# Kernel tuning notes

Hardware: AMD Instinct MI355X
Metric: run time of the kernel (lower is better)

Reference implementation:

```python
import jax, jax.numpy as jnp
import numpy as np

B, N, T, S, H = 8, 10000, 2000, 12, 128
BIN_SIGMA = 0.1
GAUSS_NORM = 0.3989422804  # 1/sqrt(2*pi), as hard-coded in the source


def setup_inputs() -> dict:
    key = jax.random.key(0)
    ks = jax.random.split(key, 8)
    # (x, y, z): x,y in detector mm, z already expressed in waveform-tick units
    scale = jnp.array([400.0, 400.0, float(T - 1)], dtype=jnp.float32)
    diffused_electrons = jax.random.uniform(ks[0], (B, N, 3), dtype=jnp.float32) * scale
    mask = jax.random.uniform(ks[1], (B, N), dtype=jnp.float32)  # per-electron weights
    W1 = jax.random.normal(ks[2], (3, H), dtype=jnp.float32) * (1.0 / np.sqrt(3.0))
    b1 = jnp.zeros((H,), dtype=jnp.float32)
    W2 = jax.random.normal(ks[3], (H, H), dtype=jnp.float32) * (1.0 / np.sqrt(H))
    b2 = jnp.zeros((H,), dtype=jnp.float32)
    W3 = jax.random.normal(ks[4], (H, S), dtype=jnp.float32) * (1.0 / np.sqrt(H))
    b3 = jnp.zeros((S,), dtype=jnp.float32)
    return {"diffused_electrons": diffused_electrons, "mask": mask,
            "W1": W1, "b1": b1, "W2": W2, "b2": b2, "W3": W3, "b3": b3}


def _mlp(x, W1, b1, W2, b2, W3, b3):
    h = jax.nn.relu(x @ W1 + b1)
    h = jaxax = jax.nn.relu(h @ W2 + b2)
    return h @ W3 + b3


def reference(diffused_electrons, mask, W1, b1, W2, b2, W3, b3):
    # sensor_simulator: per-electron sensor response [B, N, S]
    h = jax.nn.relu(diffused_electrons @ W1 + b1)
    h = jax.nn.relu(h @ W2 + b2)
    response = h @ W3 + b3  # [B, N, S]

    z = diffused_electrons[:, :, 2]  # [B, N]
    ticks = jnp.arange(T, dtype=diffused_electrons.dtype)  # linspace(0, T-1, T)
    # Gaussian soft-binning kernel, [B, N, T] (the large HBM intermediate)
    d = ticks[None, None, :] - z[:, :, None]
    exp_values = jnp.exp(-(d * d) / (2.0 * BIN_SIGMA))
    exp_values = exp_values * (mask * (GAUSS_NORM / np.sqrt(BIN_SIGMA)))[:, :, None]
    # transpose().matmul(sensor_response) then transpose -> [B, S, T]
    waveforms = jnp.einsum('bnt,bns->bst', exp_values, response)
    return waveforms
```

## Files before the change

### kernel.cpp

```cpp
#include <hip/hip_runtime.h>
#include <hip/hip_fp16.h>

#define BB 8
#define NN 10000
#define TT 2000
#define SS 12
#define HH 128
#define TOTAL_E (BB * NN)
#define COEF 1.2615662610100802f

#define CAP 32
#define REC_F 16

#define WS_CURSOR 0
#define WS_REC    65536

typedef _Float16 half8 __attribute__((ext_vector_type(8)));
typedef float f32x4 __attribute__((ext_vector_type(4)));

__device__ __forceinline__ int swz(int row, int chunk) {
    return row * 128 + ((chunk ^ (row & 7)) * 8);
}

__global__ __launch_bounds__(256) void mlp_kernel(
    const float* __restrict__ de,
    const float* __restrict__ mask,
    const float* __restrict__ W1, const float* __restrict__ b1,
    const float* __restrict__ W2, const float* __restrict__ b2,
    const float* __restrict__ W3, const float* __restrict__ b3,
    unsigned int* __restrict__ cursor,
    float* __restrict__ rec)
{
    __shared__ _Float16 sW2T[HH * 128];
    __shared__ _Float16 sh[64 * 128];

    const int tid = threadIdx.x;
    const int wave = tid >> 6;
    const int lane = tid & 63;
    const int q = lane >> 4;
    const int i = lane & 15;

    {
        const int n = tid >> 1;
        const int kh = (tid & 1) * 8;
        #pragma unroll
        for (int c8 = 0; c8 < 8; ++c8) {
            const int c = kh + c8;
            half8 v;
            #pragma unroll
            for (int j = 0; j < 8; ++j)
                v[j] = (_Float16)W2[(c * 8 + j) * HH + n];
            *(half8*)(sW2T + swz(n, c)) = v;
        }
    }

    half8 bW1[8];
    #pragma unroll
    for (int nt = 0; nt < 8; ++nt) {
        half8 f = {};
        if (q == 0) {
            const int n = nt * 16 + i;
            f[0] = (_Float16)W1[n];
            f[1] = (_Float16)W1[HH + n];
            f[2] = (_Float16)W1[2 * HH + n];
        }
        bW1[nt] = f;
    }
    half8 bW3[4];
    #pragma unroll
    for (int c = 0; c < 4; ++c) {
        half8 f = {};
        if (i < SS) {
            #pragma unroll
            for (int j = 0; j < 8; ++j)
                f[j] = (_Float16)W3[(c * 32 + q * 8 + j) * SS + i];
        }
        bW3[c] = f;
    }
    float b1v[8], b2v[8];
    #pragma unroll
    for (int nt = 0; nt < 8; ++nt) {
        b1v[nt] = b1[nt * 16 + i];
        b2v[nt] = b2[nt * 16 + i];
    }
    const float b3v = (i < SS) ? b3[i] : 0.f;

    __syncthreads();

    const int mrow = wave * 16;

    for (int base = blockIdx.x * 64; base < TOTAL_E; base += gridDim.x * 64) {
        const int m_glob = base + mrow + i;
        const int bi = m_glob / NN;
        const float x0 = de[m_glob * 3 + 0];
        const float x1 = de[m_glob * 3 + 1];
        const float x2 = de[m_glob * 3 + 2];
        const float coef = mask[m_glob] * COEF;

        half8 aX = {};
        if (q == 0) { aX[0] = (_Float16)x0; aX[1] = (_Float16)x1; aX[2] = (_Float16)x2; }

        #pragma unroll
        for (int nt = 0; nt < 8; ++nt) {
            f32x4 acc = {};
            acc = __builtin_amdgcn_mfma_f32_16x16x32_f16(aX, bW1[nt], acc, 0, 0, 0);
            #pragma unroll
            for (int r = 0; r < 4; ++r) {
                float v = acc[r] + b1v[nt];
                v = v > 0.f ? v : 0.f;
                const int row = mrow + q * 4 + r;
                const int col = nt * 16 + i;
                sh[swz(row, col >> 3) + (col & 7)] = (_Float16)v;
            }
        }
        __syncthreads();

        half8 aH[4];
        #pragma unroll
        for (int c = 0; c < 4; ++c)
            aH[c] = *(const half8*)(sh + swz(mrow + i, c * 4 + q));
        __syncthreads();

        f32x4 acc2[8];
        #pragma unroll
        for (int nt = 0; nt < 8; ++nt) acc2[nt] = (f32x4){};
        #pragma unroll
        for (int nt = 0; nt < 8; ++nt) {
            #pragma unroll
            for (int c = 0; c < 4; ++c) {
                half8 bf = *(const half8*)(sW2T + swz(nt * 16 + i, c * 4 + q));
                acc2[nt] = __builtin_amdgcn_mfma_f32_16x16x32_f16(aH[c], bf, acc2[nt], 0, 0, 0);
            }
        }
        #pragma unroll
        for (int nt = 0; nt < 8; ++nt) {
            #pragma unroll
            for (int r = 0; r < 4; ++r) {
                float v = acc2[nt][r] + b2v[nt];
                v = v > 0.f ? v : 0.f;
                const int row = mrow + q * 4 + r;
                const int col = nt * 16 + i;
                sh[swz(row, col >> 3) + (col & 7)] = (_Float16)v;
            }
        }
        __syncthreads();

        f32x4 acc3 = {};
        #pragma unroll
        for (int c = 0; c < 4; ++c) {
            half8 a2 = *(const half8*)(sh + swz(mrow + i, c * 4 + q));
            acc3 = __builtin_amdgcn_mfma_f32_16x16x32_f16(a2, bW3[c], acc3, 0, 0, 0);
        }

        unsigned int ridx = 0;
        if (lane < 16) {
            int bin = (int)x2;
            bin = bin < 0 ? 0 : (bin > TT - 1 ? TT - 1 : bin);
            unsigned int slot = atomicAdd(&cursor[bi * TT + bin], 1u);
            if (slot >= CAP) slot = CAP - 1;
            ridx = (unsigned int)(bi * TT + bin) * CAP + slot;
        }

        #pragma unroll
        for (int r = 0; r < 4; ++r) {
            const int e = q * 4 + r;
            const unsigned int rx = __shfl(ridx, e);
            const float zr = __shfl(x2, e);
            const float cr = __shfl(coef, e);
            float val;
            int f;
            if (i < SS)       { val = acc3[r] + b3v; f = 2 + i; }
            else if (i == 12) { val = zr;            f = 0; }
            else              { val = cr;            f = 1; }
            if (i < 14)
                rec[(size_t)rx * REC_F + f] = val;
        }
        __syncthreads();
    }
}

__global__ __launch_bounds__(256) void gather_kernel(
    const unsigned int* __restrict__ cursor,
    const float* __restrict__ rec,
    float* __restrict__ out)
{
    const int gid = blockIdx.x * blockDim.x + threadIdx.x;
    const int t = gid % TT;
    const int s = (gid / TT) % SS;
    const int b = gid / (TT * SS);

    int lo = t - 3; if (lo < 0) lo = 0;
    int hi = t + 3; if (hi > TT - 1) hi = TT - 1;

    const float tf = (float)t;
    float acc = 0.f;
    for (int bin = lo; bin <= hi; ++bin) {
        unsigned int cnt = cursor[b * TT + bin];
        if (cnt > CAP) cnt = CAP;
        const float* rb = rec + (size_t)(b * TT + bin) * CAP * REC_F;
        for (unsigned int u = 0; u < cnt; ++u) {
            const float* r = rb + u * REC_F;
            const float2 zc = *(const float2*)r;
            const float d = tf - zc.x;
            acc = fmaf(__expf(-5.0f * d * d) * zc.y, r[2 + s], acc);
        }
    }
    out[(b * SS + s) * TT + t] = acc;
}

extern "C" void kernel_launch(void* const* d_in, const int* in_sizes, int n_in,
                              void* d_out, int out_size, void* d_ws, size_t ws_size,
                              hipStream_t stream) {
    const float* de   = (const float*)d_in[0];
    const float* mask = (const float*)d_in[1];
    const float* W1   = (const float*)d_in[2];
    const float* b1   = (const float*)d_in[3];
    const float* W2   = (const float*)d_in[4];
    const float* b2   = (const float*)d_in[5];
    const float* W3   = (const float*)d_in[6];
    const float* b3   = (const float*)d_in[7];
    float* out = (float*)d_out;

    char* ws = (char*)d_ws;
    unsigned int* cursor = (unsigned int*)(ws + WS_CURSOR);
    float*        rec    = (float*)(ws + WS_REC);

    hipMemsetAsync(cursor, 0, BB * TT * sizeof(unsigned int), stream);

    mlp_kernel<<<625, 256, 0, stream>>>(de, mask, W1, b1, W2, b2, W3, b3,
                                        cursor, rec);
    gather_kernel<<<(BB * SS * TT) / 256, 256, 0, stream>>>(cursor, rec, out);
}
```

Before: 126.7 us.

## Pack responses as fp16 pairs and stage bin records in shared memory for gather

The per-electron record shrinks from 16 floats to 8 by packing the 12 sensor responses into six half2 words. The gather kernel now gives each block a tile of 20 ticks for all sensors. The block cooperatively loads the 26 neighbouring bins' records into LDS once, then each thread accumulates from shared memory, instead of every (t,s) thread re-reading global records. This cuts record write and read traffic and redundant global loads, at the cost of fp16 precision on the responses and 16 of 256 threads sitting idle.

```diff
diff --git a/kernel.cpp b/kernel.cpp
--- a/kernel.cpp
+++ b/kernel.cpp
@@ -10,7 +10,10 @@
 #define COEF 1.2615662610100802f
 
 #define CAP 32
-#define REC_F 16
+#define REC_W 8
+
+#define TB 20
+#define NB 26
 
 #define WS_CURSOR 0
 #define WS_REC    65536
@@ -167,13 +170,20 @@
             const unsigned int rx = __shfl(ridx, e);
             const float zr = __shfl(x2, e);
             const float cr = __shfl(coef, e);
-            float val;
-            int f;
-            if (i < SS)       { val = acc3[r] + b3v; f = 2 + i; }
-            else if (i == 12) { val = zr;            f = 0; }
-            else              { val = cr;            f = 1; }
-            if (i < 14)
-                rec[(size_t)rx * REC_F + f] = val;
+            float val = acc3[r] + b3v;
+            float val_hi = __shfl(val, lane + 1);
+            float dv = 0.f;
+            int f = -1;
+            if (i < 12 && !(i & 1)) {
+                __half2 h2;
+                h2.x = __float2half(val);
+                h2.y = __float2half(val_hi);
+                dv = *(float*)&h2;
+                f = 2 + (i >> 1);
+            } else if (i == 12) { dv = zr; f = 0; }
+            else if (i == 13)   { dv = cr; f = 1; }
+            if (f >= 0)
+                rec[(size_t)rx * REC_W + f] = dv;
         }
         __syncthreads();
     }
@@ -184,25 +194,58 @@
     const float* __restrict__ rec,
     float* __restrict__ out)
 {
-    const int gid = blockIdx.x * blockDim.x + threadIdx.x;
-    const int t = gid % TT;
-    const int s = (gid / TT) % SS;
-    const int b = gid / (TT * SS);
-
-    int lo = t - 3; if (lo < 0) lo = 0;
-    int hi = t + 3; if (hi > TT - 1) hi = TT - 1;
-
+    __shared__ float sz[NB * CAP];
+    __shared__ float sc[NB * CAP];
+    __shared__ unsigned int srsp[NB * CAP * 6];
+    __shared__ unsigned int lcnt[NB];
+
+    const int b = blockIdx.x / (TT / TB);
+    const int t0 = (blockIdx.x % (TT / TB)) * TB;
+    const int tid = threadIdx.x;
+    const int wv = tid >> 6;
+    const int ln = tid & 63;
+
+    for (int bb = wv; bb < NB; bb += 4) {
+        const int g = t0 - 3 + bb;
+        unsigned int c = 0;
+        if (g >= 0 && g < TT) {
+            c = cursor[b * TT + g];
+            if (c > CAP) c = CAP;
+        }
+        if (ln == 0) lcnt[bb] = c;
+        const float* src = rec + (size_t)(b * TT + g) * CAP * REC_W;
+        for (unsigned int idx = ln; idx < c * 8u; idx += 64) {
+            const unsigned int slot = idx >> 3;
+            const unsigned int w = idx & 7;
+            const float v = src[slot * REC_W + w];
+            const int ls = bb * CAP + slot;
+            if (w == 0)      sz[ls] = v;
+            else if (w == 1) sc[ls] = v;
+            else             srsp[ls * 6 + (w - 2)] = __float_as_uint(v);
+        }
+    }
+    __syncthreads();
+
+    const int t_l = tid / SS;
+    const int s = tid - t_l * SS;
+    if (t_l >= TB) return;
+    const int t = t0 + t_l;
     const float tf = (float)t;
     float acc = 0.f;
-    for (int bin = lo; bin <= hi; ++bin) {
-        unsigned int cnt = cursor[b * TT + bin];
-        if (cnt > CAP) cnt = CAP;
-        const float* rb = rec + (size_t)(b * TT + bin) * CAP * REC_F;
-        for (unsigned int u = 0; u < cnt; ++u) {
-            const float* r = rb + u * REC_F;
-            const float2 zc = *(const float2*)r;
-            const float d = tf - zc.x;
-            acc = fmaf(__expf(-5.0f * d * d) * zc.y, r[2 + s], acc);
+    #pragma unroll
+    for (int o = 0; o < 7; ++o) {
+        const int bb = t_l + o;
+        const unsigned int c = lcnt[bb];
+        const int base = bb * CAP;
+        for (unsigned int u = 0; u < c; ++u) {
+            const int ls = base + u;
+            const float z = sz[ls];
+            const float cc = sc[ls];
+            const float d = tf - z;
+            const unsigned int rw = srsp[ls * 6 + (s >> 1)];
+            const __half2 h2 = *(const __half2*)&rw;
+            const float rv = (s & 1) ? __half2float(h2.y) : __half2float(h2.x);
+            acc = fmaf(__expf(-5.0f * d * d) * cc, rv, acc);
         }
     }
     out[(b * SS + s) * TT + t] = acc;
@@ -229,5 +272,5 @@
 
     mlp_kernel<<<625, 256, 0, stream>>>(de, mask, W1, b1, W2, b2, W3, b3,
                                         cursor, rec);
-    gather_kernel<<<(BB * SS * TT) / 256, 256, 0, stream>>>(cursor, rec, out);
-}
+    gather_kernel<<<BB * (TT / TB), 256, 0, stream>>>(cursor, rec, out);
+}
```

Measured after the change: 106.3 us (median of 2 runs). 16.1% less time.
